# Kernel tuning notes

Measured on AMD Instinct MI355X. Metric: run time of the kernel, lower is better.

## Reference

```python
import jax, jax.numpy as jnp
import numpy as np

B, L, D, H = 4, 2048, 1024, 16
d = D // H  # head_dim = 64
EPS = 1e-5
ROPE_BASE = 10000.0


def _rope_tables(seq_len, dim):
    inv_freq = 1.0 / (ROPE_BASE ** (jnp.arange(0, dim, 2, dtype=jnp.float32) / dim))
    t = jnp.arange(seq_len, dtype=jnp.float32)
    freqs = jnp.outer(t, inv_freq)                  # (L, d/2)
    emb = jnp.concatenate([freqs, freqs], axis=-1)  # (L, d)
    return jnp.cos(emb), jnp.sin(emb)


def _rotate_half(x):
    x1, x2 = jnp.split(x, 2, axis=-1)
    return jnp.concatenate([-x2, x1], axis=-1)


def setup_inputs() -> dict:
    key = jax.random.key(0)
    ks = jax.random.split(key, 5)
    x = jax.random.normal(ks[0], (B, L, D), dtype=jnp.float32)
    attn_mask = jnp.ones((B, 1, L, L), dtype=jnp.float32)
    conversion_mask = jax.random.uniform(ks[1], (B, L), dtype=jnp.float32)
    Wqkuv = jax.random.normal(ks[2], (D, 4 * D), dtype=jnp.float32) * (1.0 / np.sqrt(D))
    Wout = jax.random.normal(ks[3], (D, D), dtype=jnp.float32) * (1.0 / np.sqrt(D))
    ln_gamma = jnp.ones((d,), dtype=jnp.float32)
    ln_beta = jnp.zeros((d,), dtype=jnp.float32)
    conv_bias = jax.random.normal(ks[4], (H,), dtype=jnp.float32) * 0.02
    return {"x": x, "attn_mask": attn_mask, "conversion_mask": conversion_mask,
            "Wqkuv": Wqkuv, "Wout": Wout, "ln_gamma": ln_gamma,
            "ln_beta": ln_beta, "conv_bias": conv_bias}


def reference(x, attn_mask, conversion_mask, Wqkuv, Wout, ln_gamma, ln_beta, conv_bias):
    # qkuv projection with SiLU
    qkuv = jax.nn.silu(jnp.einsum('bld,de->ble', x, Wqkuv))  # (B, L, 4D)
    q, k, v, u = jnp.split(qkuv, 4, axis=-1)
    # reshape to (B, H, L, d)
    to_heads = lambda t: t.reshape(B, L, H, d).transpose(0, 2, 1, 3)
    q, k, v, u = map(to_heads, (q, k, v, u))
    # RoPE
    cos, sin = _rope_tables(L, d)            # (L, d)
    cos = cos[None, None]                    # (1,1,L,d)
    sin = sin[None, None]
    q = q * cos + _rotate_half(q) * sin
    k = k * cos + _rotate_half(k) * sin
    # scores + conversion bias + SiLU + multiplicative mask
    scores = jnp.einsum('bhld,bhmd->bhlm', q, k) / jnp.sqrt(jnp.float32(d))
    scores = scores + conversion_mask[:, None, None, :] * conv_bias[None, :, None, None]
    scores = jax.nn.silu(scores)
    scores = scores * attn_mask
    # attend, LayerNorm over head_dim, SiLU-gate with u
    attn_out = jnp.einsum('bhlm,bhmd->bhld', scores, v)
    mu = jnp.mean(attn_out, axis=-1, keepdims=True)
    var = jnp.var(attn_out, axis=-1, keepdims=True)
    attn_out = (attn_out - mu) / jnp.sqrt(var + EPS) * ln_gamma + ln_beta
    attn_out = attn_out * u
    attn_out = attn_out.transpose(0, 2, 1, 3).reshape(B, L, D)
    return jnp.einsum('bld,de->ble', attn_out, Wout)
```

## Files before the change

kernel.cpp:

```cpp
#include <hip/hip_runtime.h>
#include <math.h>
#include <stdint.h>

#define B_ 4
#define L_ 2048
#define D_ 1024
#define H_ 16

typedef __attribute__((ext_vector_type(4))) float f32x4;
typedef __attribute__((ext_vector_type(2))) float f32x2;
typedef __attribute__((ext_vector_type(8))) short s16x8;
typedef __attribute__((ext_vector_type(4))) short s16x4;
typedef __attribute__((ext_vector_type(4))) unsigned short u16x4;
typedef __attribute__((ext_vector_type(4))) unsigned int u32x4;
typedef __attribute__((ext_vector_type(2))) __bf16 bf16x2;

__device__ __forceinline__ unsigned short f2bf(float f) {
  unsigned int u = __float_as_uint(f);
  u += 0x7fffu + ((u >> 16) & 1u);
  return (unsigned short)(u >> 16);
}
__device__ __forceinline__ float b2f(unsigned short s) {
  return __uint_as_float(((unsigned int)s) << 16);
}
__device__ __forceinline__ unsigned int pk2(float a, float b) {
  f32x2 v;
  v[0] = a;
  v[1] = b;
  bf16x2 r = __builtin_convertvector(v, bf16x2);
  return __builtin_bit_cast(unsigned int, r);
}
__device__ __forceinline__ float silu_fast(float v) {
  return v * __builtin_amdgcn_rcpf(1.0f + __expf(-v));
}
__device__ __forceinline__ void gl_lds16(const void* g, void* l) {
  __builtin_amdgcn_global_load_lds(
      (__attribute__((address_space(1))) void*)(uintptr_t)g,
      (__attribute__((address_space(3))) void*)(uint32_t)(uintptr_t)l, 16, 0, 0);
}

__global__ __launch_bounds__(256) void conv_x(const float* __restrict__ x,
                                              unsigned short* __restrict__ xb, int n4) {
  int i = blockIdx.x * 256 + threadIdx.x;
  if (i < n4) {
    f32x4 v = *(const f32x4*)(x + (size_t)i * 4);
    u16x4 o;
#pragma unroll
    for (int j = 0; j < 4; ++j) o[j] = f2bf(v[j]);
    *(u16x4*)(xb + (size_t)i * 4) = o;
  }
}

__global__ __launch_bounds__(256) void trans_w(const float* __restrict__ W,
                                               unsigned short* __restrict__ Wt,
                                               int K, int N) {
  __shared__ float T[64][65];
  const int k0 = blockIdx.y * 64, n0 = blockIdx.x * 64;
  const int tid = threadIdx.x;
#pragma unroll
  for (int i = 0; i < 16; ++i) {
    int e = tid + i * 256;
    int r = e >> 6, c = e & 63;
    T[r][c] = W[(size_t)(k0 + r) * N + n0 + c];
  }
  __syncthreads();
#pragma unroll
  for (int i = 0; i < 16; ++i) {
    int e = tid + i * 256;
    int r = e >> 6, c = e & 63;
    Wt[(size_t)(n0 + r) * K + k0 + c] = f2bf(T[c][r]);
  }
}

__global__ __launch_bounds__(256) void rope_tab(f32x2* __restrict__ tab) {
  int i = blockIdx.x * 256 + threadIdx.x;
  int l = i >> 5, j = i & 31;
  float inv = expf(-(float)j * (9.210340371976184f / 32.0f));
  float ang = (float)l * inv;
  f32x2 cs;
  cs[0] = cosf(ang);
  cs[1] = sinf(ang);
  tab[i] = cs;
}

template <int MODE>
__global__ __launch_bounds__(512) void gemm_bf16(const unsigned short* __restrict__ A,
                                                 const unsigned short* __restrict__ Bt,
                                                 void* __restrict__ Cp,
                                                 int M, int N, int K) {
  alignas(16) __shared__ unsigned short Ash[2][256][64];
  alignas(16) __shared__ unsigned short Bsh[2][256][64];
  const int tid = threadIdx.x;
  const int lane = tid & 63, w = tid >> 6;
  const int quad = lane >> 4, l15 = lane & 15;
  const int wm = w >> 2, wn = w & 3;
  const int nwg = gridDim.x * gridDim.y;
  const int wgid = blockIdx.y * gridDim.x + blockIdx.x;
  const int swz = (wgid & 7) * (nwg >> 3) + (wgid >> 3);
  const int m0 = (swz / gridDim.x) * 256, n0 = (swz % gridDim.x) * 256;

  const int s_sub = lane >> 3;
  const int s_src = (lane & 7) ^ s_sub;
  auto stage = [&](const unsigned short* __restrict__ G, int row0, int k0,
                   unsigned short (*dst)[64]) {
#pragma unroll
    for (int j = 0; j < 4; ++j) {
      int r = j * 64 + w * 8 + s_sub;
      gl_lds16(G + (size_t)(row0 + r) * K + k0 + s_src * 8, &dst[j * 64 + w * 8][0]);
    }
  };

  f32x4 acc[8][4] = {};
  const int NT = K / 64;

  stage(A, m0, 0, Ash[0]);
  stage(Bt, n0, 0, Bsh[0]);
  asm volatile("s_waitcnt vmcnt(0)" ::: "memory");
  __builtin_amdgcn_s_barrier();
  __builtin_amdgcn_sched_barrier(0);

  for (int t = 0; t < NT; ++t) {
    const int c = t & 1;
#pragma unroll
    for (int p = 0; p < 4; ++p) {
      const int qa = p & 1, qb = p >> 1;
      s16x8 af[4][2], bf[2][2];
#pragma unroll
      for (int i = 0; i < 4; ++i)
#pragma unroll
        for (int ks = 0; ks < 2; ++ks)
          af[i][ks] = *(const s16x8*)&Ash[c][wm * 128 + (qa * 4 + i) * 16 + l15]
                                           [((ks * 4 + quad) ^ (l15 & 7)) * 8];
#pragma unroll
      for (int jn = 0; jn < 2; ++jn)
#pragma unroll
        for (int ks = 0; ks < 2; ++ks)
          bf[jn][ks] = *(const s16x8*)&Bsh[c][wn * 64 + (qb * 2 + jn) * 16 + l15]
                                            [((ks * 4 + quad) ^ (l15 & 7)) * 8];
      if (t + 1 < NT) {
        if (p == 0) stage(A, m0, (t + 1) * 64, Ash[c ^ 1]);
        if (p == 1) stage(Bt, n0, (t + 1) * 64, Bsh[c ^ 1]);
      }
      __builtin_amdgcn_sched_barrier(0);
      __builtin_amdgcn_s_barrier();
      __builtin_amdgcn_sched_barrier(0);
      __builtin_amdgcn_s_setprio(1);
#pragma unroll
      for (int i = 0; i < 4; ++i)
#pragma unroll
        for (int jn = 0; jn < 2; ++jn)
#pragma unroll
          for (int ks = 0; ks < 2; ++ks)
            acc[qa * 4 + i][qb * 2 + jn] = __builtin_amdgcn_mfma_f32_16x16x32_bf16(
                af[i][ks], bf[jn][ks], acc[qa * 4 + i][qb * 2 + jn], 0, 0, 0);
      __builtin_amdgcn_s_setprio(0);
      if (p < 3) {
        __builtin_amdgcn_s_barrier();
        __builtin_amdgcn_sched_barrier(0);
      }
    }
    if (t + 1 < NT) {
      asm volatile("s_waitcnt vmcnt(0)" ::: "memory");
    }
    __builtin_amdgcn_s_barrier();
    __builtin_amdgcn_sched_barrier(0);
  }

#pragma unroll
  for (int fm = 0; fm < 8; ++fm)
#pragma unroll
    for (int fn = 0; fn < 4; ++fn)
#pragma unroll
      for (int reg = 0; reg < 4; ++reg) {
        int rg = m0 + wm * 128 + fm * 16 + quad * 4 + reg;
        int cg = n0 + wn * 64 + fn * 16 + l15;
        float v = acc[fm][fn][reg];
        if (MODE == 1) {
          ((unsigned short*)Cp)[(size_t)rg * N + cg] = f2bf(silu_fast(v));
        } else {
          ((float*)Cp)[(size_t)rg * N + cg] = v;
        }
      }
}

__global__ __launch_bounds__(256) void rope_conv(unsigned short* __restrict__ qk,
                                                 unsigned short* __restrict__ vt,
                                                 const f32x2* __restrict__ tab) {
  alignas(16) __shared__ unsigned short Vsh[64][72];
  const int tid = threadIdx.x;
  const int bh = blockIdx.y, b = bh >> 4, h = bh & 15;
  const int l0 = blockIdx.x * 64;
#pragma unroll
  for (int i = 0; i < 2; ++i) {
    int p = tid + i * 256;
    int row = p >> 3, c4 = p & 7;
    int l = l0 + row;
    size_t base = (size_t)(b * L_ + l) * 4096 + h * 64 + c4 * 4;
#pragma unroll
    for (int t = 0; t < 2; ++t) {
      size_t o = base + (size_t)t * 1024;
      u16x4 lo = *(u16x4*)(qk + o);
      u16x4 hi = *(u16x4*)(qk + o + 32);
      u16x4 nlo, nhi;
#pragma unroll
      for (int jj = 0; jj < 4; ++jj) {
        f32x2 cs = tab[l * 32 + c4 * 4 + jj];
        float fl = b2f(lo[jj]), fh = b2f(hi[jj]);
        nlo[jj] = f2bf(fl * cs[0] - fh * cs[1]);
        nhi[jj] = f2bf(fh * cs[0] + fl * cs[1]);
      }
      *(u16x4*)(qk + o) = nlo;
      *(u16x4*)(qk + o + 32) = nhi;
    }
  }
#pragma unroll
  for (int i = 0; i < 2; ++i) {
    int ch = tid + i * 256;
    int row = ch >> 3, c8 = ch & 7;
    *(s16x8*)&Vsh[row][c8 * 8] =
        *(const s16x8*)(qk + (size_t)(b * L_ + l0 + row) * 4096 + 2048 + h * 64 + c8 * 8);
  }
  __syncthreads();
#pragma unroll
  for (int i = 0; i < 2; ++i) {
    int ch = tid + i * 256;
    int drow = ch >> 3, c8 = ch & 7;
    s16x8 o;
#pragma unroll
    for (int jj = 0; jj < 8; ++jj) {
      int pos = c8 * 8 + jj;
      int g = pos >> 5, p = pos & 31;
      int lk = g * 32 + ((p >> 2) & 1) * 16 + ((p >> 3) & 3) * 4 + (p & 3);
      o[jj] = (short)Vsh[lk][drow];
    }
    *(s16x8*)(vt + (size_t)(bh * 64 + drow) * 2048 + l0 + c8 * 8) = o;
  }
}

__global__ __launch_bounds__(256) void attn_mfma(
    const unsigned short* __restrict__ qk, const unsigned short* __restrict__ vt,
    const float* __restrict__ amask, const float* __restrict__ cmask,
    const float* __restrict__ cbias, const float* __restrict__ gamma,
    const float* __restrict__ beta, unsigned short* __restrict__ attng) {
  alignas(16) __shared__ unsigned short Ks[64][64];
  alignas(16) __shared__ unsigned short Vts[64][64];
  const int tid = threadIdx.x;
  const int lane = tid & 63, w = tid >> 6;
  const int quad = lane >> 4, l15 = lane & 15;
  const int bh = blockIdx.y, b = bh >> 4, h = bh & 15;
  const int l0 = blockIdx.x * 128;
  const float cb = cbias[h];
  const int srow = lane >> 3;
  const int schunk = (lane & 7) ^ srow;

  s16x8 qf[2][2];
  const float* abase[2];
#pragma unroll
  for (int qs = 0; qs < 2; ++qs) {
    int qg = l0 + w * 32 + qs * 16 + l15;
#pragma unroll
    for (int s = 0; s < 2; ++s)
      qf[qs][s] = *(const s16x8*)(qk + (size_t)(b * L_ + qg) * 4096 + h * 64 + s * 32 + quad * 8);
    abase[qs] = amask + ((size_t)b * L_ + qg) * L_;
  }
  const float* cbase = cmask + (size_t)b * L_;

  f32x4 oacc[2][4] = {};

  for (int m0 = 0; m0 < L_; m0 += 64) {
    __syncthreads();
#pragma unroll
    for (int i = 0; i < 2; ++i) {
      int r0 = w * 16 + i * 8;
      gl_lds16(qk + (size_t)(b * L_ + m0 + r0 + srow) * 4096 + 1024 + h * 64 + schunk * 8,
               &Ks[r0][0]);
      gl_lds16(vt + (size_t)(bh * 64 + r0 + srow) * 2048 + m0 + schunk * 8, &Vts[r0][0]);
    }
    f32x4 cmcb[4], am4[2][4];
#pragma unroll
    for (int kt = 0; kt < 4; ++kt)
      cmcb[kt] = *(const f32x4*)(cbase + m0 + kt * 16 + quad * 4) * cb;
#pragma unroll
    for (int qs = 0; qs < 2; ++qs)
#pragma unroll
      for (int kt = 0; kt < 4; ++kt)
        am4[qs][kt] = *(const f32x4*)(abase[qs] + m0 + kt * 16 + quad * 4);
    __syncthreads();

    f32x4 sacc[2][4] = {};
#pragma unroll
    for (int s = 0; s < 2; ++s) {
      s16x8 kf[4];
#pragma unroll
      for (int kt = 0; kt < 4; ++kt)
        kf[kt] = *(const s16x8*)&Ks[kt * 16 + l15][((s * 4 + quad) ^ (l15 & 7)) * 8];
      __builtin_amdgcn_s_setprio(1);
#pragma unroll
      for (int qs = 0; qs < 2; ++qs)
#pragma unroll
        for (int kt = 0; kt < 4; ++kt)
          sacc[qs][kt] = __builtin_amdgcn_mfma_f32_16x16x32_bf16(kf[kt], qf[qs][s],
                                                                 sacc[qs][kt], 0, 0, 0);
      __builtin_amdgcn_s_setprio(0);
    }

    s16x8 pf[2][2];
#pragma unroll
    for (int qs = 0; qs < 2; ++qs)
#pragma unroll
      for (int t = 0; t < 2; ++t) {
        u32x4 pw;
#pragma unroll
        for (int half = 0; half < 2; ++half) {
          int kt = 2 * t + half;
          float x[4];
#pragma unroll
          for (int r = 0; r < 4; ++r) {
            float v = fmaf(sacc[qs][kt][r], 0.125f, cmcb[kt][r]);
            v = silu_fast(v);
            x[r] = v * am4[qs][kt][r];
          }
          pw[half * 2 + 0] = pk2(x[0], x[1]);
          pw[half * 2 + 1] = pk2(x[2], x[3]);
        }
        pf[qs][t] = __builtin_bit_cast(s16x8, pw);
      }

#pragma unroll
    for (int dt = 0; dt < 4; ++dt)
#pragma unroll
      for (int t = 0; t < 2; ++t) {
        s16x8 vf = *(const s16x8*)&Vts[dt * 16 + l15][((t * 4 + quad) ^ (l15 & 7)) * 8];
        __builtin_amdgcn_s_setprio(1);
#pragma unroll
        for (int qs = 0; qs < 2; ++qs)
          oacc[qs][dt] = __builtin_amdgcn_mfma_f32_16x16x32_bf16(pf[qs][t], vf,
                                                                 oacc[qs][dt], 0, 0, 0);
        __builtin_amdgcn_s_setprio(0);
      }
  }

#pragma unroll
  for (int qs = 0; qs < 2; ++qs) {
    float sm[4], sq[4];
#pragma unroll
    for (int reg = 0; reg < 4; ++reg) {
      float s1 = 0.f, s2 = 0.f;
#pragma unroll
      for (int dt = 0; dt < 4; ++dt) {
        float v = oacc[qs][dt][reg];
        s1 += v;
        s2 += v * v;
      }
      sm[reg] = s1;
      sq[reg] = s2;
    }
#pragma unroll
    for (int m = 1; m < 16; m <<= 1) {
#pragma unroll
      for (int reg = 0; reg < 4; ++reg) {
        sm[reg] += __shfl_xor(sm[reg], m);
        sq[reg] += __shfl_xor(sq[reg], m);
      }
    }
    float mu[4], rs[4];
#pragma unroll
    for (int reg = 0; reg < 4; ++reg) {
      mu[reg] = sm[reg] * (1.0f / 64.0f);
      float var = sq[reg] * (1.0f / 64.0f) - mu[reg] * mu[reg];
      rs[reg] = rsqrtf(var + 1e-5f);
    }
#pragma unroll
    for (int dt = 0; dt < 4; ++dt) {
      float g = gamma[dt * 16 + l15], be = beta[dt * 16 + l15];
#pragma unroll
      for (int reg = 0; reg < 4; ++reg) {
        int rowg = l0 + w * 32 + qs * 16 + quad * 4 + reg;
        int colg = dt * 16 + l15;
        float v = (oacc[qs][dt][reg] - mu[reg]) * rs[reg] * g + be;
        float u = b2f(qk[(size_t)(b * L_ + rowg) * 4096 + 3072 + h * 64 + colg]);
        attng[(size_t)(b * L_ + rowg) * 1024 + h * 64 + colg] = f2bf(v * u);
      }
    }
  }
}

extern "C" void kernel_launch(void* const* d_in, const int* in_sizes, int n_in,
                              void* d_out, int out_size, void* d_ws, size_t ws_size,
                              hipStream_t stream) {
  const float* x = (const float*)d_in[0];
  const float* amask = (const float*)d_in[1];
  const float* cmask = (const float*)d_in[2];
  const float* Wqkuv = (const float*)d_in[3];
  const float* Wout = (const float*)d_in[4];
  const float* gamma = (const float*)d_in[5];
  const float* beta = (const float*)d_in[6];
  const float* cbias = (const float*)d_in[7];
  float* out = (float*)d_out;

  char* ws = (char*)d_ws;
  unsigned short* qkuv_bf = (unsigned short*)ws;
  unsigned short* vt = (unsigned short*)(ws + ((size_t)64 << 20));
  unsigned short* xbf = (unsigned short*)(ws + ((size_t)80 << 20));
  unsigned short* Wt = (unsigned short*)(ws + ((size_t)96 << 20));
  unsigned short* Wot = (unsigned short*)(ws + ((size_t)104 << 20));
  unsigned short* attng = (unsigned short*)(ws + ((size_t)106 << 20));
  f32x2* tab = (f32x2*)(ws + ((size_t)122 << 20));

  conv_x<<<8192, 256, 0, stream>>>(x, xbf, (B_ * L_ * D_) / 4);
  trans_w<<<dim3(4096 / 64, 1024 / 64), 256, 0, stream>>>(Wqkuv, Wt, 1024, 4096);
  trans_w<<<dim3(1024 / 64, 1024 / 64), 256, 0, stream>>>(Wout, Wot, 1024, 1024);
  rope_tab<<<(L_ * 32) / 256, 256, 0, stream>>>(tab);

  gemm_bf16<1><<<dim3(4096 / 256, 8192 / 256), 512, 0, stream>>>(xbf, Wt, qkuv_bf,
                                                                 B_ * L_, 4 * D_, D_);
  rope_conv<<<dim3(L_ / 64, B_ * H_), 256, 0, stream>>>(qkuv_bf, vt, tab);
  attn_mfma<<<dim3(L_ / 128, B_ * H_), 256, 0, stream>>>(qkuv_bf, vt, amask, cmask, cbias,
                                                         gamma, beta, attng);
  gemm_bf16<0><<<dim3(1024 / 256, 8192 / 256), 512, 0, stream>>>(attng, Wot, out,
                                                                 B_ * L_, D_, D_);
}
```

Measured before the change: 458.8 us.

## Split GEMM staging into quarter loads with partial waits; add 128-tile output GEMM

The 256x256 GEMM now issues its next-tile global-to-LDS loads in four pieces, one per compute phase, and waits with partial vmcnt counts instead of draining everything at the end of each k-step. This is meant to keep loads in flight while MFMAs run. Separately, the output projection moves to a new 128x128-tile, 256-thread kernel, which gives 512 workgroups instead of 128 so more CUs are busy on the small N=1024 GEMM. The new kernel has no double buffering, and the vmcnt accounting is fragile.

```diff
diff --git a/kernel.cpp b/kernel.cpp
--- a/kernel.cpp
+++ b/kernel.cpp
@@ -101,21 +101,30 @@
 
   const int s_sub = lane >> 3;
   const int s_src = (lane & 7) ^ s_sub;
-  auto stage = [&](const unsigned short* __restrict__ G, int row0, int k0,
-                   unsigned short (*dst)[64]) {
-#pragma unroll
-    for (int j = 0; j < 4; ++j) {
-      int r = j * 64 + w * 8 + s_sub;
-      gl_lds16(G + (size_t)(row0 + r) * K + k0 + s_src * 8, &dst[j * 64 + w * 8][0]);
+
+  auto stageA = [&](int k0, int qa, unsigned short(*dst)[64]) {
+#pragma unroll
+    for (int g = 0; g < 2; ++g) {
+      int rb = qa * 64 + g * 128 + w * 8;
+      gl_lds16(A + (size_t)(m0 + rb + s_sub) * K + k0 + s_src * 8, &dst[rb][0]);
+    }
+  };
+  auto stageB = [&](int k0, int qb, unsigned short(*dst)[64]) {
+#pragma unroll
+    for (int g = 0; g < 2; ++g) {
+      int rb = qb * 32 + g * 128 + (w >> 2) * 64 + (w & 3) * 8;
+      gl_lds16(Bt + (size_t)(n0 + rb + s_sub) * K + k0 + s_src * 8, &dst[rb][0]);
     }
   };
 
   f32x4 acc[8][4] = {};
   const int NT = K / 64;
 
-  stage(A, m0, 0, Ash[0]);
-  stage(Bt, n0, 0, Bsh[0]);
-  asm volatile("s_waitcnt vmcnt(0)" ::: "memory");
+  stageA(0, 0, Ash[0]);
+  stageB(0, 0, Bsh[0]);
+  stageA(0, 1, Ash[0]);
+  stageB(0, 1, Bsh[0]);
+  asm volatile("s_waitcnt vmcnt(4)" ::: "memory");
   __builtin_amdgcn_s_barrier();
   __builtin_amdgcn_sched_barrier(0);
 
@@ -138,8 +147,10 @@
           bf[jn][ks] = *(const s16x8*)&Bsh[c][wn * 64 + (qb * 2 + jn) * 16 + l15]
                                             [((ks * 4 + quad) ^ (l15 & 7)) * 8];
       if (t + 1 < NT) {
-        if (p == 0) stage(A, m0, (t + 1) * 64, Ash[c ^ 1]);
-        if (p == 1) stage(Bt, n0, (t + 1) * 64, Bsh[c ^ 1]);
+        if (p == 0) stageA((t + 1) * 64, 0, Ash[c ^ 1]);
+        if (p == 1) stageB((t + 1) * 64, 0, Bsh[c ^ 1]);
+        if (p == 2) stageA((t + 1) * 64, 1, Ash[c ^ 1]);
+        if (p == 3) stageB((t + 1) * 64, 1, Bsh[c ^ 1]);
       }
       __builtin_amdgcn_sched_barrier(0);
       __builtin_amdgcn_s_barrier();
@@ -154,16 +165,16 @@
             acc[qa * 4 + i][qb * 2 + jn] = __builtin_amdgcn_mfma_f32_16x16x32_bf16(
                 af[i][ks], bf[jn][ks], acc[qa * 4 + i][qb * 2 + jn], 0, 0, 0);
       __builtin_amdgcn_s_setprio(0);
-      if (p < 3) {
-        __builtin_amdgcn_s_barrier();
-        __builtin_amdgcn_sched_barrier(0);
-      }
-    }
-    if (t + 1 < NT) {
-      asm volatile("s_waitcnt vmcnt(0)" ::: "memory");
-    }
-    __builtin_amdgcn_s_barrier();
-    __builtin_amdgcn_sched_barrier(0);
+      __builtin_amdgcn_sched_barrier(0);
+      if (t + 1 < NT) {
+        if (p != 2) asm volatile("s_waitcnt vmcnt(4)" ::: "memory");
+      } else {
+        if (p == 0) asm volatile("s_waitcnt vmcnt(2)" ::: "memory");
+        if (p == 1) asm volatile("s_waitcnt vmcnt(0)" ::: "memory");
+      }
+      __builtin_amdgcn_s_barrier();
+      __builtin_amdgcn_sched_barrier(0);
+    }
   }
 
 #pragma unroll
@@ -175,6 +186,62 @@
         int rg = m0 + wm * 128 + fm * 16 + quad * 4 + reg;
         int cg = n0 + wn * 64 + fn * 16 + l15;
         float v = acc[fm][fn][reg];
+        if (MODE == 1) {
+          ((unsigned short*)Cp)[(size_t)rg * N + cg] = f2bf(silu_fast(v));
+        } else {
+          ((float*)Cp)[(size_t)rg * N + cg] = v;
+        }
+      }
+}
+
+template <int MODE>
+__global__ __launch_bounds__(256) void gemm128_bf16(const unsigned short* __restrict__ A,
+                                                    const unsigned short* __restrict__ Bt,
+                                                    void* __restrict__ Cp,
+                                                    int M, int N, int K) {
+  alignas(16) __shared__ unsigned short As[128][32];
+  alignas(16) __shared__ unsigned short Bs[128][32];
+  const int tid = threadIdx.x;
+  const int lane = tid & 63, w = tid >> 6;
+  const int quad = lane >> 4, l15 = lane & 15;
+  const int wr = w >> 1, wc = w & 1;
+  const int nwg = gridDim.x * gridDim.y;
+  const int wgid = blockIdx.y * gridDim.x + blockIdx.x;
+  const int swz = (wgid & 7) * (nwg >> 3) + (wgid >> 3);
+  const int m0 = (swz / gridDim.x) * 128, n0 = (swz % gridDim.x) * 128;
+  const int srow = lane >> 2;
+  const int schunk = (lane & 3) ^ ((lane >> 3) & 3);
+  const int fcol = (quad ^ ((l15 >> 1) & 3)) * 8;
+  f32x4 acc[4][4] = {};
+  for (int k0 = 0; k0 < K; k0 += 32) {
+    __syncthreads();
+#pragma unroll
+    for (int i = 0; i < 2; ++i) {
+      int r0 = (w * 2 + i) * 16;
+      gl_lds16(A + (size_t)(m0 + r0 + srow) * K + k0 + schunk * 8, &As[r0][0]);
+      gl_lds16(Bt + (size_t)(n0 + r0 + srow) * K + k0 + schunk * 8, &Bs[r0][0]);
+    }
+    __syncthreads();
+    s16x8 af[4], bf[4];
+#pragma unroll
+    for (int mi = 0; mi < 4; ++mi) af[mi] = *(const s16x8*)&As[wr * 64 + mi * 16 + l15][fcol];
+#pragma unroll
+    for (int nj = 0; nj < 4; ++nj) bf[nj] = *(const s16x8*)&Bs[wc * 64 + nj * 16 + l15][fcol];
+#pragma unroll
+    for (int mi = 0; mi < 4; ++mi)
+#pragma unroll
+      for (int nj = 0; nj < 4; ++nj)
+        acc[mi][nj] = __builtin_amdgcn_mfma_f32_16x16x32_bf16(af[mi], bf[nj], acc[mi][nj], 0, 0, 0);
+  }
+#pragma unroll
+  for (int mi = 0; mi < 4; ++mi)
+#pragma unroll
+    for (int nj = 0; nj < 4; ++nj)
+#pragma unroll
+      for (int reg = 0; reg < 4; ++reg) {
+        int rg = m0 + wr * 64 + mi * 16 + quad * 4 + reg;
+        int cg = n0 + wc * 64 + nj * 16 + l15;
+        float v = acc[mi][nj][reg];
         if (MODE == 1) {
           ((unsigned short*)Cp)[(size_t)rg * N + cg] = f2bf(silu_fast(v));
         } else {
@@ -417,6 +484,6 @@
   rope_conv<<<dim3(L_ / 64, B_ * H_), 256, 0, stream>>>(qkuv_bf, vt, tab);
   attn_mfma<<<dim3(L_ / 128, B_ * H_), 256, 0, stream>>>(qkuv_bf, vt, amask, cmask, cbias,
                                                          gamma, beta, attng);
-  gemm_bf16<0><<<dim3(1024 / 256, 8192 / 256), 512, 0, stream>>>(attng, Wot, out,
-                                                                 B_ * L_, D_, D_);
-}
+  gemm128_bf16<0><<<dim3(1024 / 128, 8192 / 128), 256, 0, stream>>>(attng, Wot, out,
+                                                                    B_ * L_, D_, D_);
+}
```

Measured after the change: 452.7 us. Within noise of the previous version (-1.3%).
